# Optimization experiments

Hardware: AMD Instinct MI355X
Metric: run time of the kernel (lower is better)

Reference implementation:

```python
import jax, jax.numpy as jnp
import numpy as np

EPS = 1e-12


def _update_side(states, left, right, layer_idx, cache_position):
    """Norm-based rank decomposition scatter update for one of K or V.

    states: [H, S, D] float32 (batch dim already squeezed)
    left:   [L, H, M, R] float16 cache buffer
    right:  [L, H, R, D] float16 cache buffer
    Semantics match the torch loop: for each head h and each position i,
      left[layer, h, pos_i, 0] = ||states[h, i]||_2, left[layer, h, pos_i, 1:] = 0
      right[layer, h]          = zeros; row 0 = normalized states of the LAST i
    (right is overwritten every iteration, so only the last position survives).
    Returns (reconstructed [1, S, ...], new_left, new_right).
    Assumes cache_position == arange(S) starting from an empty cache, so
    current_seq_len == S (static shape, jit-friendly).
    """
    H, S, D = states.shape
    R = left.shape[-1]
    # per-position L2 norms -> first rank column, rest zero
    norms = jnp.linalg.norm(states, axis=-1)                      # [H, S]
    rows = jnp.zeros((H, S, R), left.dtype).at[:, :, 0].set(norms.astype(left.dtype))
    left_layer = left[layer_idx].at[:, cache_position, :].set(rows)   # [H, M, R]
    left = left.at[layer_idx].set(left_layer)
    last = states[:, -1, :]                                       # [H, D]
    last_n = last / (jnp.linalg.norm(last, axis=-1, keepdims=True) + EPS)
    right_layer = jnp.zeros((H, R, D), right.dtype).at[:, 0, :].set(last_n.astype(right.dtype))
    right = right.at[layer_idx].set(right_layer)
    # reconstruction in fp32 over the filled prefix (current_seq_len == S)
    recon = jnp.einsum(
        'hsr,hrd->hsd',
        left[layer_idx][:, :S, :].astype(jnp.float32),
        right[layer_idx].astype(jnp.float32),
    )
    return recon[None], left, right  # [1, H, S, D]


def setup_inputs() -> dict:
    key = jax.random.key(0)
    k0, k1 = jax.random.split(key)
    L, H, M, R, D, S = 8, 32, 8192, 16, 128, 4096
    return {
        'key_states': jax.random.normal(k0, (1, H, S, D), jnp.float32),
        'value_states': jax.random.normal(k1, (1, H, S, D), jnp.float32),
        'k_left': jnp.zeros((L, H, M, R), jnp.float16),
        'k_right': jnp.zeros((L, H, R, D), jnp.float16),
        'v_left': jnp.zeros((L, H, M, R), jnp.float16),
        'v_right': jnp.zeros((L, H, R, D), jnp.float16),
        'cache_position': jnp.arange(S, dtype=jnp.int32),
        'layer_idx': 3,
    }


def reference(key_states, value_states, k_left, k_right, v_left, v_right,
              cache_position, layer_idx):
    k_full, _, _ = _update_side(key_states[0], k_left, k_right, layer_idx, cache_position)
    v_full, _, _ = _update_side(value_states[0], v_left, v_right, layer_idx, cache_position)
    return k_full, v_full
```

## Files before the change

kernel.cpp:

```cpp
#include <hip/hip_runtime.h>
#include <hip/hip_fp16.h>

constexpr int H = 32;
constexpr int S = 4096;
constexpr int D = 128;
constexpr float EPSF = 1e-12f;

typedef float vfloat4 __attribute__((ext_vector_type(4)));

__global__ void VLKV_fused_kernel(const float* __restrict__ K,
                                  const float* __restrict__ V,
                                  float* __restrict__ out) {
    const int tid  = threadIdx.x;
    const int lane = tid & 63;
    const int wv   = tid >> 6;
    const int half = lane >> 5;
    const int li   = lane & 31;

    const long w    = (long)blockIdx.x * (blockDim.x >> 6) + wv;
    const long row0 = w * 32;
    const int  side = (int)(row0 >> 17);
    const long srow0 = row0 & (long)(H * S - 1);
    const int  h    = (int)(srow0 >> 12);

    const float* base = (side == 0 ? K : V);

    const float4 lv = *(const float4*)(base + ((long)h * S + (S - 1)) * D + li * 4);
    float lss = lv.x * lv.x + lv.y * lv.y + lv.z * lv.z + lv.w * lv.w;
#pragma unroll
    for (int m = 1; m < 32; m <<= 1) lss += __shfl_xor(lss, m);
    const float inv = 1.0f / (sqrtf(lss) + EPSF);
    float4 ln;
    ln.x = __half2float(__float2half(lv.x * inv));
    ln.y = __half2float(__float2half(lv.y * inv));
    ln.z = __half2float(__float2half(lv.z * inv));
    ln.w = __half2float(__float2half(lv.w * inv));

    const float* src = base + (srow0 + half) * (long)D + li * 4;
    float*       dst = out  + (row0  + half) * (long)D + li * 4;

#pragma unroll 4
    for (int i = 0; i < 16; ++i) {
        const float4 x = *(const float4*)(src + (long)i * 2 * D);
        float ss = x.x * x.x + x.y * x.y + x.z * x.z + x.w * x.w;
#pragma unroll
        for (int m = 1; m < 32; m <<= 1) ss += __shfl_xor(ss, m);
        const float nh = __half2float(__float2half(sqrtf(ss)));

        vfloat4 o;
        o.x = nh * ln.x;
        o.y = nh * ln.y;
        o.z = nh * ln.z;
        o.w = nh * ln.w;
        __builtin_nontemporal_store(o, (vfloat4*)(dst + (long)i * 2 * D));
    }
}

extern "C" void kernel_launch(void* const* d_in, const int* in_sizes, int n_in,
                              void* d_out, int out_size, void* d_ws, size_t ws_size,
                              hipStream_t stream) {
    const float* K = (const float*)d_in[0];
    const float* V = (const float*)d_in[1];
    float* out = (float*)d_out;

    VLKV_fused_kernel<<<2048, 256, 0, stream>>>(K, V, out);
}
```

Measured before the change: 44.81 us.

## Split fused kernel into separate norm-compute and output-write kernels

Replaces the single fused read-reduce-write kernel with two launches. The first reads K/V and stores per-row half-rounded norms to workspace, and the second reads only norms and the last row to write the output. The intent is to separate the read-bound and write-bound phases so each streams cleanly. It adds a second launch and a small workspace round trip, and falls back to the fused kernel when workspace is too small.

```diff
diff --git a/kernel.cpp b/kernel.cpp
--- a/kernel.cpp
+++ b/kernel.cpp
@@ -5,8 +5,83 @@
 constexpr int S = 4096;
 constexpr int D = 128;
 constexpr float EPSF = 1e-12f;
+constexpr long NROWS = 2L * H * S;
 
 typedef float vfloat4 __attribute__((ext_vector_type(4)));
+
+__global__ void VLKV_norms_kernel(const float* __restrict__ K,
+                                  const float* __restrict__ V,
+                                  float* __restrict__ norms) {
+    const int tid  = threadIdx.x;
+    const int lane = tid & 63;
+    const int wv   = tid >> 6;
+    const int half = lane >> 5;
+    const int li   = lane & 31;
+
+    const long w     = (long)blockIdx.x * (blockDim.x >> 6) + wv;
+    const long row0  = w * 32;
+    const int  side  = (int)(row0 >> 17);
+    const long srow0 = row0 & (long)(H * S - 1);
+
+    const float* src = (side == 0 ? K : V) + (srow0 + half) * (long)D + li * 4;
+
+#pragma unroll 4
+    for (int i = 0; i < 16; ++i) {
+        const float4 x = *(const float4*)(src + (long)i * 2 * D);
+        float ss = x.x * x.x + x.y * x.y + x.z * x.z + x.w * x.w;
+#pragma unroll
+        for (int m = 1; m < 32; m <<= 1) ss += __shfl_xor(ss, m);
+        if (li == 0) {
+            norms[row0 + i * 2 + half] =
+                __half2float(__float2half(sqrtf(ss)));
+        }
+    }
+}
+
+__global__ void VLKV_write_kernel(const float* __restrict__ K,
+                                  const float* __restrict__ V,
+                                  const float* __restrict__ norms,
+                                  float* __restrict__ out) {
+    const int tid  = threadIdx.x;
+    const int lane = tid & 63;
+    const int wv   = tid >> 6;
+    const int half = lane >> 5;
+    const int li   = lane & 31;
+
+    const long w     = (long)blockIdx.x * (blockDim.x >> 6) + wv;
+    const long row0  = w * 32;
+    const int  side  = (int)(row0 >> 17);
+    const long srow0 = row0 & (long)(H * S - 1);
+    const int  h     = (int)(srow0 >> 12);
+
+    const float* base = (side == 0 ? K : V);
+
+    const float4 lv = *(const float4*)(base + ((long)h * S + (S - 1)) * D + li * 4);
+    float lss = lv.x * lv.x + lv.y * lv.y + lv.z * lv.z + lv.w * lv.w;
+#pragma unroll
+    for (int m = 1; m < 32; m <<= 1) lss += __shfl_xor(lss, m);
+    const float inv = 1.0f / (sqrtf(lss) + EPSF);
+    float4 ln;
+    ln.x = __half2float(__float2half(lv.x * inv));
+    ln.y = __half2float(__float2half(lv.y * inv));
+    ln.z = __half2float(__float2half(lv.z * inv));
+    ln.w = __half2float(__float2half(lv.w * inv));
+
+    const float nv = norms[row0 + (lane & 31)];
+
+    float* dst = out + (row0 + half) * (long)D + li * 4;
+
+#pragma unroll 8
+    for (int i = 0; i < 16; ++i) {
+        const float nh = __shfl(nv, i * 2 + half);
+        vfloat4 o;
+        o.x = nh * ln.x;
+        o.y = nh * ln.y;
+        o.z = nh * ln.z;
+        o.w = nh * ln.w;
+        __builtin_nontemporal_store(o, (vfloat4*)(dst + (long)i * 2 * D));
+    }
+}
 
 __global__ void VLKV_fused_kernel(const float* __restrict__ K,
                                   const float* __restrict__ V,
@@ -17,11 +92,11 @@
     const int half = lane >> 5;
     const int li   = lane & 31;
 
-    const long w    = (long)blockIdx.x * (blockDim.x >> 6) + wv;
-    const long row0 = w * 32;
-    const int  side = (int)(row0 >> 17);
+    const long w     = (long)blockIdx.x * (blockDim.x >> 6) + wv;
+    const long row0  = w * 32;
+    const int  side  = (int)(row0 >> 17);
     const long srow0 = row0 & (long)(H * S - 1);
-    const int  h    = (int)(srow0 >> 12);
+    const int  h     = (int)(srow0 >> 12);
 
     const float* base = (side == 0 ? K : V);
 
@@ -46,7 +121,6 @@
 #pragma unroll
         for (int m = 1; m < 32; m <<= 1) ss += __shfl_xor(ss, m);
         const float nh = __half2float(__float2half(sqrtf(ss)));
-
         vfloat4 o;
         o.x = nh * ln.x;
         o.y = nh * ln.y;
@@ -63,5 +137,12 @@
     const float* V = (const float*)d_in[1];
     float* out = (float*)d_out;
 
-    VLKV_fused_kernel<<<2048, 256, 0, stream>>>(K, V, out);
+    const size_t norms_bytes = (size_t)NROWS * sizeof(float);
+    if (ws_size >= norms_bytes) {
+        float* norms = (float*)d_ws;
+        VLKV_norms_kernel<<<2048, 256, 0, stream>>>(K, V, norms);
+        VLKV_write_kernel<<<2048, 256, 0, stream>>>(K, V, norms, out);
+    } else {
+        VLKV_fused_kernel<<<2048, 256, 0, stream>>>(K, V, out);
+    }
 }
```

After: 50.58 us. 12.9% more time.
